# Optimization experiments

Hardware: AMD Instinct MI355X
Metric: run time of the kernel (lower is better)

## Reference

```python
import jax, jax.numpy as jnp
import numpy as np

N = 100000   # nodes
E = 1600000  # edges
IN = 128     # input feature dim
HID = 64     # hidden = IN // 2
OUT = 8      # output_size
B = 16384    # lookup batch


def sage_conv(x, src, dst, W_l, W_r, b, n):
    # PyG SAGEConv (aggr='mean', root_weight=True):
    # out = lin_l(mean_{j in N(i)} x_j) + lin_r(x_i)
    msgs = x[src]                                              # [E, F] gather
    agg = jax.ops.segment_sum(msgs, dst, num_segments=n)       # [N, F] scatter-add
    deg = jax.ops.segment_sum(jnp.ones((src.shape[0],), x.dtype), dst, num_segments=n)
    mean = agg / jnp.maximum(deg, 1.0)[:, None]                # zero-degree -> 0
    return mean @ W_l + x @ W_r + b


def setup_inputs() -> dict:
    key = jax.random.key(0)
    ks = jax.random.split(key, 10)
    node_feats = jax.random.normal(ks[0], (N, IN), dtype=jnp.float32)
    edge_index = jax.random.randint(ks[1], (2, E), 0, N, dtype=jnp.int64)
    idx = jax.random.randint(ks[2], (B,), 0, N, dtype=jnp.int64)
    dropout_mask = jax.random.uniform(ks[3], (N, HID), dtype=jnp.float32)
    s1 = 1.0 / np.sqrt(IN)
    s2 = 1.0 / np.sqrt(HID)
    W1_l = jax.random.normal(ks[4], (IN, HID), dtype=jnp.float32) * s1
    W1_r = jax.random.normal(ks[5], (IN, HID), dtype=jnp.float32) * s1
    b1 = jnp.zeros((HID,), dtype=jnp.float32)
    W2_l = jax.random.normal(ks[6], (HID, OUT), dtype=jnp.float32) * s2
    W2_r = jax.random.normal(ks[7], (HID, OUT), dtype=jnp.float32) * s2
    b2 = jnp.zeros((OUT,), dtype=jnp.float32)
    return {"node_feats": node_feats, "edge_index": edge_index, "idx": idx,
            "dropout_mask": dropout_mask, "W1_l": W1_l, "W1_r": W1_r, "b1": b1,
            "W2_l": W2_l, "W2_r": W2_r, "b2": b2}


def reference(node_feats, edge_index, idx, dropout_mask, W1_l, W1_r, b1, W2_l, W2_r, b2):
    n = node_feats.shape[0]
    src, dst = edge_index[0], edge_index[1]
    h = sage_conv(node_feats, src, dst, W1_l, W1_r, b1, n)     # [N, HID]
    h = jax.nn.relu(h)
    keep = (dropout_mask > 0.5).astype(h.dtype)                # F.dropout p=0.5
    h = h * keep * 2.0                                         # inverted dropout scale 1/(1-p)
    emb = sage_conv(h, src, dst, W2_l, W2_r, b2, n)            # [N, OUT]
    return emb[idx]                                            # [B, OUT]
```

## Files before the change

### kernel.cpp

```cpp
#include <hip/hip_runtime.h>
#include <hip/hip_fp16.h>

#define IN_F 128
#define HID_F 64
#define OUT_F 8

#define BSHIFT 7
#define BGRAN 128
#define BCAP 2688
#define NBUK_MAX 784
#define CHUNK 4096
#define EPT (CHUNK / 256)
#define CEPT ((BCAP + 255) / 256)

typedef _Float16 f16x8 __attribute__((ext_vector_type(8)));
typedef float f32x4 __attribute__((ext_vector_type(4)));

__global__ __launch_bounds__(256) void prep(
    const float* __restrict__ Wl, const float* __restrict__ Wr,
    _Float16* __restrict__ Wt, int* __restrict__ bcur, int nbuk) {
  int blk = blockIdx.x;
  if (blk < 16) {
    int i = blk * 256 + threadIdx.x;
    int n = i & 127;
    int k4 = (i >> 7) * 4;
    _Float16 hv[4];
#pragma unroll
    for (int j = 0; j < 4; ++j) {
      float v = (n < HID_F) ? Wl[(k4 + j) * HID_F + n]
                            : Wr[(k4 + j) * HID_F + (n - HID_F)];
      hv[j] = (_Float16)v;
    }
    *(uint2*)(Wt + (size_t)n * IN_F + k4) = *(uint2*)hv;
  } else {
    for (int i = threadIdx.x; i < nbuk; i += 256) bcur[i] = i * BCAP;
  }
}

__global__ __launch_bounds__(256) void bucket_scatter(
    const int* __restrict__ src, const int* __restrict__ dst,
    int* __restrict__ bcur, int* __restrict__ ebuf,
    const float* __restrict__ mask, unsigned long long* __restrict__ mbits,
    int n_edges, int n_nodes) {
  __shared__ int hist[NBUK_MAX];
  __shared__ int base[NBUK_MAX];
  int t = threadIdx.x;
  for (int i = t; i < NBUK_MAX; i += 256) hist[i] = 0;
  __syncthreads();
  int e0 = blockIdx.x * CHUNK;
  int pk[EPT];
  int bk[EPT];
  int rk[EPT];
#pragma unroll
  for (int k = 0; k < EPT; ++k) {
    int e = e0 + k * 256 + t;
    if (e < n_edges) {
      int s = src[e];
      int d = dst[e];
      bk[k] = d >> BSHIFT;
      pk[k] = ((d & (BGRAN - 1)) << 24) | s;
      rk[k] = atomicAdd(&hist[bk[k]], 1);
    } else {
      bk[k] = -1;
    }
  }
  __syncthreads();
  for (int i = t; i < NBUK_MAX; i += 256) {
    int c = hist[i];
    base[i] = c ? atomicAdd(&bcur[i], c) : 0;
  }
  __syncthreads();
#pragma unroll
  for (int k = 0; k < EPT; ++k) {
    if (bk[k] >= 0) ebuf[base[bk[k]] + rk[k]] = pk[k];
  }

  int mpb = (n_nodes + (int)gridDim.x - 1) / (int)gridDim.x;
  int nb0 = blockIdx.x * mpb;
  int lim = min(nb0 + mpb, n_nodes);
  int w = t >> 6;
  int ln = t & 63;
  for (int nn = nb0 + w * 4; nn < lim; nn += 16) {
    float m0 = (nn + 0 < lim) ? mask[(size_t)(nn + 0) * HID_F + ln] : 0.f;
    float m1 = (nn + 1 < lim) ? mask[(size_t)(nn + 1) * HID_F + ln] : 0.f;
    float m2 = (nn + 2 < lim) ? mask[(size_t)(nn + 2) * HID_F + ln] : 0.f;
    float m3 = (nn + 3 < lim) ? mask[(size_t)(nn + 3) * HID_F + ln] : 0.f;
    unsigned long long b0 = __ballot(m0 > 0.5f);
    unsigned long long b1 = __ballot(m1 > 0.5f);
    unsigned long long b2 = __ballot(m2 > 0.5f);
    unsigned long long b3 = __ballot(m3 > 0.5f);
    if (ln == 0) {
      if (nn + 0 < lim) mbits[nn + 0] = b0;
      if (nn + 1 < lim) mbits[nn + 1] = b1;
      if (nn + 2 < lim) mbits[nn + 2] = b2;
      if (nn + 3 < lim) mbits[nn + 3] = b3;
    }
  }
}

__global__ __launch_bounds__(256) void bucket_csr(
    const int* __restrict__ ebuf, const int* __restrict__ bcur,
    uint2* __restrict__ nd, int* __restrict__ csr_src, int n_nodes) {
  __shared__ int hist[BGRAN];
  __shared__ int excl_s[BGRAN];
  __shared__ int lds_src[BCAP];
  int b = blockIdx.x;
  int t = threadIdx.x;
  if (t < BGRAN) hist[t] = 0;
  __syncthreads();
  int beg = b * BCAP;
  int cnt = bcur[b] - beg;
  int pk[CEPT];
  int rk[CEPT];
#pragma unroll
  for (int u = 0; u < CEPT; ++u) {
    int j = t + u * 256;
    if (j < cnt) {
      pk[u] = ebuf[beg + j];
      rk[u] = atomicAdd(&hist[(unsigned)pk[u] >> 24], 1);
    } else {
      pk[u] = -1;
    }
  }
  __syncthreads();
  if (t < 64) {
    int h0 = hist[2 * t];
    int h1 = hist[2 * t + 1];
    int ps = h0 + h1;
#pragma unroll
    for (int dd = 1; dd < 64; dd <<= 1) {
      int u = __shfl_up(ps, dd);
      if (t >= dd) ps += u;
    }
    excl_s[2 * t] = ps - h1 - h0;
    excl_s[2 * t + 1] = ps - h1;
  }
  __syncthreads();
  if (t < BGRAN) {
    int node = b * BGRAN + t;
    if (node < n_nodes)
      nd[node] = make_uint2((unsigned)(beg + excl_s[t]), (unsigned)hist[t]);
  }
#pragma unroll
  for (int u = 0; u < CEPT; ++u) {
    if (pk[u] != -1) {
      int bin = (unsigned)pk[u] >> 24;
      lds_src[excl_s[bin] + rk[u]] = pk[u] & 0xFFFFFF;
    }
  }
  __syncthreads();
  for (int j = t; j < cnt; j += 256) csr_src[beg + j] = lds_src[j];
}

#define K1_ROWS 64
#define XSH 136
__global__ __launch_bounds__(256) void k1_proj(
    const float* __restrict__ x,
    const _Float16* __restrict__ Wt,
    const float* __restrict__ b1,
    __half* __restrict__ y1h,
    __half* __restrict__ r1h,
    int n_nodes) {
  __shared__ _Float16 XS[K1_ROWS * XSH];
  int tid = threadIdx.x;
  int w = tid >> 6;
  int lane = tid & 63;
  int n0 = blockIdx.x * K1_ROWS;
  int m = lane & 15;
  int quad = lane >> 4;

  f16x8 af[2][4];
#pragma unroll
  for (int ti = 0; ti < 2; ++ti) {
    int t = w + ti * 4;
#pragma unroll
    for (int kk = 0; kk < 4; ++kk)
      af[ti][kk] = *(const f16x8*)(Wt + (size_t)(t * 16 + m) * IN_F + kk * 32 + quad * 8);
  }
  float4 b1v = *(const float4*)(b1 + w * 16 + quad * 4);

#pragma unroll
  for (int p = 0; p < 8; ++p) {
    int i = tid + p * 256;
    int row = i >> 5;
    int k4 = (i & 31) * 4;
    int gs = min(n0 + row, n_nodes - 1);
    float4 v = *(const float4*)(x + (size_t)gs * IN_F + k4);
    _Float16 hv[4] = {(_Float16)v.x, (_Float16)v.y, (_Float16)v.z, (_Float16)v.w};
    *(uint2*)&XS[row * XSH + k4] = *(uint2*)hv;
  }
  __syncthreads();

#pragma unroll
  for (int rt = 0; rt < 4; ++rt) {
    f32x4 acc0 = f32x4{0.f, 0.f, 0.f, 0.f};
    f32x4 acc1 = f32x4{0.f, 0.f, 0.f, 0.f};
#pragma unroll
    for (int kk = 0; kk < 4; ++kk) {
      f16x8 bx = *(const f16x8*)&XS[(rt * 16 + m) * XSH + kk * 32 + quad * 8];
      acc0 = __builtin_amdgcn_mfma_f32_16x16x32_f16(af[0][kk], bx, acc0, 0, 0, 0);
      acc1 = __builtin_amdgcn_mfma_f32_16x16x32_f16(af[1][kk], bx, acc1, 0, 0, 0);
    }
    int node = n0 + rt * 16 + m;
    if (node < n_nodes) {
      __half hy[4], hr[4];
#pragma unroll
      for (int r = 0; r < 4; ++r) {
        hy[r] = __float2half(acc0[r]);
        hr[r] = __float2half(acc1[r] + ((const float*)&b1v)[r]);
      }
      *(uint2*)(y1h + (size_t)node * HID_F + w * 16 + quad * 4) = *(uint2*)hy;
      *(uint2*)(r1h + (size_t)node * HID_F + w * 16 + quad * 4) = *(uint2*)hr;
    }
  }
}

__global__ __launch_bounds__(256) void agg1_fused(
    const __half* __restrict__ y1h,
    const __half* __restrict__ r1h,
    const uint2* __restrict__ nd,
    const int* __restrict__ csr_src,
    const unsigned long long* __restrict__ mbits,
    __half* __restrict__ h_h,
    int n_nodes, int npw) {
  int wid = (blockIdx.x * 256 + threadIdx.x) >> 6;
  int lane = threadIdx.x & 63;
  int q = lane >> 4;
  int f4 = lane & 15;
  int n0 = wid * npw;
  if (n0 >= n_nodes) return;
  int nend = min(n0 + npw, n_nodes);
  const char* yb = (const char*)y1h;
  unsigned foff = (unsigned)(f4 * 8);

#define ACCB(g0, g1, g2, g3)                                 \
  {                                                          \
    __half2 hx = *(const __half2*)&(g0).x;                   \
    __half2 hy = *(const __half2*)&(g0).y;                   \
    hx = __hadd2(hx, *(const __half2*)&(g1).x);              \
    hy = __hadd2(hy, *(const __half2*)&(g1).y);              \
    hx = __hadd2(hx, *(const __half2*)&(g2).x);              \
    hy = __hadd2(hy, *(const __half2*)&(g2).y);              \
    hx = __hadd2(hx, *(const __half2*)&(g3).x);              \
    hy = __hadd2(hy, *(const __half2*)&(g3).y);              \
    float2 fx = __half22float2(hx);                          \
    float2 fy = __half22float2(hy);                          \
    a0 += fx.x; a1 += fx.y; a2 += fy.x; a3 += fy.y;          \
  }

  int nu0 = __builtin_amdgcn_readfirstlane(n0);
  uint2 be_c = nd[nu0];
  unsigned pidx[4] = {0u, 0u, 0u, 0u};
  {
    int d0 = (int)be_c.y;
    if (d0 > 0) {
      const int* cp0 = csr_src + (int)be_c.x;
      int dm = d0 - 1;
#pragma unroll
      for (int k = 0; k < 4; ++k)
        pidx[k] = (unsigned)cp0[min(4 * k + q, dm)];
    }
  }

  for (int n = n0; n < nend; ++n) {
    int nu = __builtin_amdgcn_readfirstlane(n);
    unsigned long long mb = mbits[nu];
    size_t o = (size_t)nu * HID_F + f4 * 4;
    uint2 rg = *(const uint2*)(r1h + o);
    uint2 be_n = make_uint2(0u, 0u);
    if (n + 1 < nend) {
      int nun = __builtin_amdgcn_readfirstlane(n + 1);
      be_n = nd[nun];
    }

    int d = (int)be_c.y;
    const int* cp = csr_src + (int)be_c.x;
    float a0 = 0.f, a1 = 0.f, a2 = 0.f, a3 = 0.f;

    if (d > 0) {
      uint2 g0 = *(const uint2*)(yb + ((pidx[0] << 7) + foff));
      uint2 g1 = *(const uint2*)(yb + ((pidx[1] << 7) + foff));
      uint2 g2 = *(const uint2*)(yb + ((pidx[2] << 7) + foff));
      uint2 g3 = *(const uint2*)(yb + ((pidx[3] << 7) + foff));
      uint2 zz = make_uint2(0u, 0u);
      if (q >= d) g0 = zz;
      if (4 + q >= d) g1 = zz;
      if (8 + q >= d) g2 = zz;
      if (12 + q >= d) g3 = zz;
      ACCB(g0, g1, g2, g3)
    }
    int j = 16;
    for (; j + 16 <= d; j += 16) {
      unsigned s0 = (unsigned)cp[j + q];
      unsigned s1 = (unsigned)cp[j + 4 + q];
      unsigned s2 = (unsigned)cp[j + 8 + q];
      unsigned s3 = (unsigned)cp[j + 12 + q];
      uint2 g0 = *(const uint2*)(yb + ((s0 << 7) + foff));
      uint2 g1 = *(const uint2*)(yb + ((s1 << 7) + foff));
      uint2 g2 = *(const uint2*)(yb + ((s2 << 7) + foff));
      uint2 g3 = *(const uint2*)(yb + ((s3 << 7) + foff));
      ACCB(g0, g1, g2, g3)
    }
    if (j < d) {
      int dm = d - 1;
      int e0 = j + q, e1 = j + 4 + q, e2 = j + 8 + q, e3 = j + 12 + q;
      unsigned s0 = (unsigned)cp[min(e0, dm)];
      unsigned s1 = (unsigned)cp[min(e1, dm)];
      unsigned s2 = (unsigned)cp[min(e2, dm)];
      unsigned s3 = (unsigned)cp[min(e3, dm)];
      uint2 g0 = *(const uint2*)(yb + ((s0 << 7) + foff));
      uint2 g1 = *(const uint2*)(yb + ((s1 << 7) + foff));
      uint2 g2 = *(const uint2*)(yb + ((s2 << 7) + foff));
      uint2 g3 = *(const uint2*)(yb + ((s3 << 7) + foff));
      uint2 zz = make_uint2(0u, 0u);
      if (e0 >= d) g0 = zz;
      if (e1 >= d) g1 = zz;
      if (e2 >= d) g2 = zz;
      if (e3 >= d) g3 = zz;
      ACCB(g0, g1, g2, g3)
    }

    if (n + 1 < nend) {
      int dn = (int)be_n.y;
      if (dn > 0) {
        const int* cpn = csr_src + (int)be_n.x;
        int dmn = dn - 1;
#pragma unroll
        for (int k = 0; k < 4; ++k)
          pidx[k] = (unsigned)cpn[min(4 * k + q, dmn)];
      }
    }

    a0 += __shfl_xor(a0, 16); a0 += __shfl_xor(a0, 32);
    a1 += __shfl_xor(a1, 16); a1 += __shfl_xor(a1, 32);
    a2 += __shfl_xor(a2, 16); a2 += __shfl_xor(a2, 32);
    a3 += __shfl_xor(a3, 16); a3 += __shfl_xor(a3, 32);
    if (q == 0) {
      float inv = 1.0f / fmaxf((float)d, 1.0f);
      float2 r01 = __half22float2(*(const __half2*)&rg.x);
      float2 r23 = __half22float2(*(const __half2*)&rg.y);
      float vx = fmaxf(a0 * inv + r01.x, 0.f);
      float vy = fmaxf(a1 * inv + r01.y, 0.f);
      float vz = fmaxf(a2 * inv + r23.x, 0.f);
      float vw = fmaxf(a3 * inv + r23.y, 0.f);
      int fb = f4 * 4;
      vx = ((mb >> (fb + 0)) & 1ull) ? vx * 2.f : 0.f;
      vy = ((mb >> (fb + 1)) & 1ull) ? vy * 2.f : 0.f;
      vz = ((mb >> (fb + 2)) & 1ull) ? vz * 2.f : 0.f;
      vw = ((mb >> (fb + 3)) & 1ull) ? vw * 2.f : 0.f;
      __half hh[4] = {__float2half(vx), __float2half(vy),
                      __float2half(vz), __float2half(vw)};
      *(uint2*)(h_h + o) = *(uint2*)hh;
    }
    be_c = be_n;
  }
#undef ACCB
}

__global__ __launch_bounds__(256) void k3b_z(
    const __half* __restrict__ h_h,
    const float* __restrict__ W2l,
    __half* __restrict__ z,
    int n_nodes) {
  __shared__ float WS[HID_F][OUT_F];
  int tid = threadIdx.x;
  if (tid < 128) {
    float4 w = *(const float4*)(W2l + tid * 4);
    *(float4*)&WS[tid >> 1][(tid & 1) * 4] = w;
  }
  __syncthreads();
  int node = blockIdx.x * blockDim.x + tid;
  if (node >= n_nodes) return;
  const __half* hr = h_h + (size_t)node * HID_F;
  float acc[8] = {0, 0, 0, 0, 0, 0, 0, 0};
  for (int k = 0; k < HID_F; k += 8) {
    uint4 hv = *(const uint4*)(hr + k);
    float2 f0 = __half22float2(*(const __half2*)&hv.x);
    float2 f1 = __half22float2(*(const __half2*)&hv.y);
    float2 f2 = __half22float2(*(const __half2*)&hv.z);
    float2 f3 = __half22float2(*(const __half2*)&hv.w);
    float hh[8] = {f0.x, f0.y, f1.x, f1.y, f2.x, f2.y, f3.x, f3.y};
#pragma unroll
    for (int j = 0; j < 8; ++j) {
      float4 w0 = *(const float4*)&WS[k + j][0];
      float4 w1 = *(const float4*)&WS[k + j][4];
      acc[0] += hh[j] * w0.x; acc[1] += hh[j] * w0.y;
      acc[2] += hh[j] * w0.z; acc[3] += hh[j] * w0.w;
      acc[4] += hh[j] * w1.x; acc[5] += hh[j] * w1.y;
      acc[6] += hh[j] * w1.z; acc[7] += hh[j] * w1.w;
    }
  }
  __half hz[8];
#pragma unroll
  for (int j = 0; j < 8; ++j) hz[j] = __float2half(acc[j]);
  *(uint4*)(z + (size_t)node * OUT_F) = *(uint4*)hz;
}

__global__ __launch_bounds__(256) void out_fused(
    const int* __restrict__ idx,
    const __half* __restrict__ z,
    const uint2* __restrict__ nd,
    const int* __restrict__ csr_src,
    const __half* __restrict__ h_h,
    const float* __restrict__ W2r,
    const float* __restrict__ b2,
    float* __restrict__ out,
    int n_batch) {
  int b = (blockIdx.x * blockDim.x + threadIdx.x) >> 6;
  int lane = threadIdx.x & 63;
  if (b >= n_batch) return;
  int bu = __builtin_amdgcn_readfirstlane(b);
  int i = idx[bu];
  int iu = __builtin_amdgcn_readfirstlane(i);
  int e8 = lane >> 3;
  int o = lane & 7;
  uint2 be = nd[iu];
  uint4 hv = *(const uint4*)(h_h + (size_t)iu * HID_F + e8 * 8);
  int beg = (int)be.x;
  int d = (int)be.y;
  const int* cp = csr_src + beg;
  const char* zb = (const char*)z;
  unsigned ooff = (unsigned)(o * 2);
  float acc = 0.f;
  int j = e8;
  for (; j + 8 < d; j += 16) {
    unsigned s0 = (unsigned)cp[j];
    unsigned s1 = (unsigned)cp[j + 8];
    float z0 = __half2float(*(const __half*)(zb + ((s0 << 4) + ooff)));
    float z1 = __half2float(*(const __half*)(zb + ((s1 << 4) + ooff)));
    acc += z0 + z1;
  }
  if (j < d) {
    unsigned s0 = (unsigned)cp[j];
    acc += __half2float(*(const __half*)(zb + ((s0 << 4) + ooff)));
  }
  float dv = fmaxf((float)d, 1.0f);
  float v = acc / dv;
  float2 f0 = __half22float2(*(const __half2*)&hv.x);
  float2 f1 = __half22float2(*(const __half2*)&hv.y);
  float2 f2 = __half22float2(*(const __half2*)&hv.z);
  float2 f3 = __half22float2(*(const __half2*)&hv.w);
  float hh[8] = {f0.x, f0.y, f1.x, f1.y, f2.x, f2.y, f3.x, f3.y};
#pragma unroll
  for (int jj = 0; jj < 8; ++jj) {
    int k = e8 * 8 + jj;
    v += hh[jj] * W2r[k * OUT_F + o];
  }
  v += __shfl_xor(v, 8);
  v += __shfl_xor(v, 16);
  v += __shfl_xor(v, 32);
  if (e8 == 0) out[(size_t)b * OUT_F + o] = v + b2[o];
}

extern "C" void kernel_launch(void* const* d_in, const int* in_sizes, int n_in,
                              void* d_out, int out_size, void* d_ws, size_t ws_size,
                              hipStream_t stream) {
  const float* x    = (const float*)d_in[0];
  const int*   ei   = (const int*)d_in[1];
  const int*   idx  = (const int*)d_in[2];
  const float* mask = (const float*)d_in[3];
  const float* W1l  = (const float*)d_in[4];
  const float* W1r  = (const float*)d_in[5];
  const float* b1   = (const float*)d_in[6];
  const float* W2l  = (const float*)d_in[7];
  const float* W2r  = (const float*)d_in[8];
  const float* b2   = (const float*)d_in[9];
  float* out = (float*)d_out;

  int n_nodes = in_sizes[0] / IN_F;
  int n_edges = in_sizes[1] / 2;
  int n_batch = in_sizes[2];
  const int* src = ei;
  const int* dst = ei + n_edges;

  int nbuk = (n_nodes + BGRAN - 1) / BGRAN;
  int nchunk = (n_edges + CHUNK - 1) / CHUNK;

  char* ws = (char*)d_ws;
  size_t off = 0;
  __half* y1h = (__half*)(ws + off); off += (size_t)n_nodes * HID_F * 2;
  __half* r1h = (__half*)(ws + off); off += (size_t)n_nodes * HID_F * 2;
  __half* h_h = (__half*)(ws + off); off += (size_t)n_nodes * HID_F * 2;
  __half* z   = (__half*)(ws + off); off += (size_t)n_nodes * OUT_F * 2;
  unsigned long long* mbits = (unsigned long long*)(ws + off); off += (size_t)n_nodes * 8;
  _Float16* Wt = (_Float16*)(ws + off); off += (size_t)IN_F * IN_F * 2;
  int* ebuf    = (int*)(ws + off); off += (size_t)nbuk * BCAP * 4;
  int* csr_src = (int*)(ws + off); off += (size_t)nbuk * BCAP * 4;
  uint2* nd    = (uint2*)(ws + off); off += (size_t)n_nodes * 8;
  int* bcur    = (int*)(ws + off); off += NBUK_MAX * 4;

  prep<<<17, 256, 0, stream>>>(W1l, W1r, Wt, bcur, nbuk);
  bucket_scatter<<<nchunk, 256, 0, stream>>>(src, dst, bcur, ebuf,
                                             mask, mbits, n_edges, n_nodes);
  k1_proj<<<(n_nodes + K1_ROWS - 1) / K1_ROWS, 256, 0, stream>>>(
      x, Wt, b1, y1h, r1h, n_nodes);
  bucket_csr<<<nbuk, 256, 0, stream>>>(ebuf, bcur, nd, csr_src, n_nodes);

  {
    int tw = 8192;
    int npw = (n_nodes + tw - 1) / tw;
    int nw = (n_nodes + npw - 1) / npw;
    int blocks = (nw + 3) / 4;
    agg1_fused<<<blocks, 256, 0, stream>>>(
        y1h, r1h, nd, csr_src, mbits, h_h, n_nodes, npw);
  }

  k3b_z<<<(n_nodes + 255) / 256, 256, 0, stream>>>(h_h, W2l, z, n_nodes);
  {
    long long th = (long long)n_batch * 64;
    out_fused<<<(int)((th + 255) / 256), 256, 0, stream>>>(
        idx, z, nd, csr_src, h_h, W2r, b2, out, n_batch);
  }
}
```

Measured before the change: 236.3 us.

## Process two nodes per wave in agg1 and move mask packing to bucket_csr

Result: slower. 247.6 us (+4.8%).

```diff
diff --git a/kernel.cpp b/kernel.cpp
--- a/kernel.cpp
+++ b/kernel.cpp
@@ -9,7 +9,7 @@
 #define BGRAN 128
 #define BCAP 2688
 #define NBUK_MAX 784
-#define CHUNK 4096
+#define CHUNK 2048
 #define EPT (CHUNK / 256)
 #define CEPT ((BCAP + 255) / 256)
 
@@ -39,9 +39,7 @@
 
 __global__ __launch_bounds__(256) void bucket_scatter(
     const int* __restrict__ src, const int* __restrict__ dst,
-    int* __restrict__ bcur, int* __restrict__ ebuf,
-    const float* __restrict__ mask, unsigned long long* __restrict__ mbits,
-    int n_edges, int n_nodes) {
+    int* __restrict__ bcur, int* __restrict__ ebuf, int n_edges) {
   __shared__ int hist[NBUK_MAX];
   __shared__ int base[NBUK_MAX];
   int t = threadIdx.x;
@@ -74,33 +72,13 @@
   for (int k = 0; k < EPT; ++k) {
     if (bk[k] >= 0) ebuf[base[bk[k]] + rk[k]] = pk[k];
   }
-
-  int mpb = (n_nodes + (int)gridDim.x - 1) / (int)gridDim.x;
-  int nb0 = blockIdx.x * mpb;
-  int lim = min(nb0 + mpb, n_nodes);
-  int w = t >> 6;
-  int ln = t & 63;
-  for (int nn = nb0 + w * 4; nn < lim; nn += 16) {
-    float m0 = (nn + 0 < lim) ? mask[(size_t)(nn + 0) * HID_F + ln] : 0.f;
-    float m1 = (nn + 1 < lim) ? mask[(size_t)(nn + 1) * HID_F + ln] : 0.f;
-    float m2 = (nn + 2 < lim) ? mask[(size_t)(nn + 2) * HID_F + ln] : 0.f;
-    float m3 = (nn + 3 < lim) ? mask[(size_t)(nn + 3) * HID_F + ln] : 0.f;
-    unsigned long long b0 = __ballot(m0 > 0.5f);
-    unsigned long long b1 = __ballot(m1 > 0.5f);
-    unsigned long long b2 = __ballot(m2 > 0.5f);
-    unsigned long long b3 = __ballot(m3 > 0.5f);
-    if (ln == 0) {
-      if (nn + 0 < lim) mbits[nn + 0] = b0;
-      if (nn + 1 < lim) mbits[nn + 1] = b1;
-      if (nn + 2 < lim) mbits[nn + 2] = b2;
-      if (nn + 3 < lim) mbits[nn + 3] = b3;
-    }
-  }
 }
 
 __global__ __launch_bounds__(256) void bucket_csr(
     const int* __restrict__ ebuf, const int* __restrict__ bcur,
-    uint2* __restrict__ nd, int* __restrict__ csr_src, int n_nodes) {
+    uint2* __restrict__ nd, int* __restrict__ csr_src,
+    const float* __restrict__ mask, unsigned long long* __restrict__ mbits,
+    int n_nodes) {
   __shared__ int hist[BGRAN];
   __shared__ int excl_s[BGRAN];
   __shared__ int lds_src[BCAP];
@@ -150,6 +128,31 @@
   }
   __syncthreads();
   for (int j = t; j < cnt; j += 256) csr_src[beg + j] = lds_src[j];
+
+  {
+    int w = t >> 6;
+    int ln = t & 63;
+    int nb0 = b * BGRAN + w * 32;
+    int nlim = min(b * BGRAN + BGRAN, n_nodes);
+#pragma unroll
+    for (int u = 0; u < 8; ++u) {
+      int nn = nb0 + u * 4;
+      float m0 = (nn + 0 < nlim) ? mask[(size_t)(nn + 0) * HID_F + ln] : 0.f;
+      float m1 = (nn + 1 < nlim) ? mask[(size_t)(nn + 1) * HID_F + ln] : 0.f;
+      float m2 = (nn + 2 < nlim) ? mask[(size_t)(nn + 2) * HID_F + ln] : 0.f;
+      float m3 = (nn + 3 < nlim) ? mask[(size_t)(nn + 3) * HID_F + ln] : 0.f;
+      unsigned long long b0 = __ballot(m0 > 0.5f);
+      unsigned long long b1 = __ballot(m1 > 0.5f);
+      unsigned long long b2 = __ballot(m2 > 0.5f);
+      unsigned long long b3 = __ballot(m3 > 0.5f);
+      if (ln == 0) {
+        if (nn + 0 < nlim) mbits[nn + 0] = b0;
+        if (nn + 1 < nlim) mbits[nn + 1] = b1;
+        if (nn + 2 < nlim) mbits[nn + 2] = b2;
+        if (nn + 3 < nlim) mbits[nn + 3] = b3;
+      }
+    }
+  }
 }
 
 #define K1_ROWS 64
@@ -212,6 +215,97 @@
       *(uint2*)(y1h + (size_t)node * HID_F + w * 16 + quad * 4) = *(uint2*)hy;
       *(uint2*)(r1h + (size_t)node * HID_F + w * 16 + quad * 4) = *(uint2*)hr;
     }
+  }
+}
+
+__device__ __forceinline__ void load_pidx(unsigned* pidx, uint2 be,
+                                          const int* __restrict__ csr_src,
+                                          int q) {
+  int dd = (int)be.y;
+  if (dd > 0) {
+    const int* cp_ = csr_src + (int)be.x;
+    int dm_ = dd - 1;
+#pragma unroll
+    for (int k = 0; k < 8; ++k)
+      pidx[k] = (unsigned)cp_[min(4 * k + q, dm_)];
+  } else {
+#pragma unroll
+    for (int k = 0; k < 8; ++k) pidx[k] = 0u;
+  }
+}
+
+__device__ __forceinline__ void gather8(uint2* g, const unsigned* pidx,
+                                        const char* __restrict__ yb,
+                                        unsigned foff, int d) {
+  uint2 zz = make_uint2(0u, 0u);
+#pragma unroll
+  for (int k = 0; k < 4; ++k)
+    g[k] = *(const uint2*)(yb + ((pidx[k] << 7) + foff));
+  if (d > 16) {
+#pragma unroll
+    for (int k = 4; k < 8; ++k)
+      g[k] = *(const uint2*)(yb + ((pidx[k] << 7) + foff));
+  } else {
+#pragma unroll
+    for (int k = 4; k < 8; ++k) g[k] = zz;
+  }
+}
+
+__device__ __forceinline__ void accum8(const uint2* g, int d, int q,
+                                       float& a0, float& a1,
+                                       float& a2, float& a3) {
+  unsigned zi = 0u;
+  __half2 hx = *(const __half2*)&zi;
+  __half2 hy = *(const __half2*)&zi;
+#pragma unroll
+  for (int k = 0; k < 4; ++k) {
+    uint2 gk = (4 * k + q < d) ? g[k] : make_uint2(0u, 0u);
+    hx = __hadd2(hx, *(const __half2*)&gk.x);
+    hy = __hadd2(hy, *(const __half2*)&gk.y);
+  }
+  float2 fx = __half22float2(hx);
+  float2 fy = __half22float2(hy);
+  a0 += fx.x; a1 += fx.y; a2 += fy.x; a3 += fy.y;
+  if (d > 16) {
+    __half2 ux = *(const __half2*)&zi;
+    __half2 uy = *(const __half2*)&zi;
+#pragma unroll
+    for (int k = 4; k < 8; ++k) {
+      uint2 gk = (4 * k + q < d) ? g[k] : make_uint2(0u, 0u);
+      ux = __hadd2(ux, *(const __half2*)&gk.x);
+      uy = __hadd2(uy, *(const __half2*)&gk.y);
+    }
+    float2 gx = __half22float2(ux);
+    float2 gy = __half22float2(uy);
+    a0 += gx.x; a1 += gx.y; a2 += gy.x; a3 += gy.y;
+  }
+}
+
+__device__ __forceinline__ void reduce_epi(float a0, float a1, float a2,
+                                           float a3, int d, uint2 rg,
+                                           unsigned long long mb, size_t o,
+                                           int q, int f4,
+                                           __half* __restrict__ h_h) {
+  a0 += __shfl_xor(a0, 16); a0 += __shfl_xor(a0, 32);
+  a1 += __shfl_xor(a1, 16); a1 += __shfl_xor(a1, 32);
+  a2 += __shfl_xor(a2, 16); a2 += __shfl_xor(a2, 32);
+  a3 += __shfl_xor(a3, 16); a3 += __shfl_xor(a3, 32);
+  if (q == 0) {
+    float inv = 1.0f / fmaxf((float)d, 1.0f);
+    float2 r01 = __half22float2(*(const __half2*)&rg.x);
+    float2 r23 = __half22float2(*(const __half2*)&rg.y);
+    float vx = fmaxf(a0 * inv + r01.x, 0.f);
+    float vy = fmaxf(a1 * inv + r01.y, 0.f);
+    float vz = fmaxf(a2 * inv + r23.x, 0.f);
+    float vw = fmaxf(a3 * inv + r23.y, 0.f);
+    int fb = f4 * 4;
+    vx = ((mb >> (fb + 0)) & 1ull) ? vx * 2.f : 0.f;
+    vy = ((mb >> (fb + 1)) & 1ull) ? vy * 2.f : 0.f;
+    vz = ((mb >> (fb + 2)) & 1ull) ? vz * 2.f : 0.f;
+    vw = ((mb >> (fb + 3)) & 1ull) ? vw * 2.f : 0.f;
+    __half hh[4] = {__float2half(vx), __float2half(vy),
+                    __float2half(vz), __float2half(vw)};
+    *(uint2*)(h_h + o) = *(uint2*)hh;
   }
 }
 
@@ -233,128 +327,122 @@
   const char* yb = (const char*)y1h;
   unsigned foff = (unsigned)(f4 * 8);
 
-#define ACCB(g0, g1, g2, g3)                                 \
-  {                                                          \
-    __half2 hx = *(const __half2*)&(g0).x;                   \
-    __half2 hy = *(const __half2*)&(g0).y;                   \
-    hx = __hadd2(hx, *(const __half2*)&(g1).x);              \
-    hy = __hadd2(hy, *(const __half2*)&(g1).y);              \
-    hx = __hadd2(hx, *(const __half2*)&(g2).x);              \
-    hy = __hadd2(hy, *(const __half2*)&(g2).y);              \
-    hx = __hadd2(hx, *(const __half2*)&(g3).x);              \
-    hy = __hadd2(hy, *(const __half2*)&(g3).y);              \
-    float2 fx = __half22float2(hx);                          \
-    float2 fy = __half22float2(hy);                          \
-    a0 += fx.x; a1 += fx.y; a2 += fy.x; a3 += fy.y;          \
-  }
-
-  int nu0 = __builtin_amdgcn_readfirstlane(n0);
-  uint2 be_c = nd[nu0];
-  unsigned pidx[4] = {0u, 0u, 0u, 0u};
-  {
-    int d0 = (int)be_c.y;
-    if (d0 > 0) {
-      const int* cp0 = csr_src + (int)be_c.x;
-      int dm = d0 - 1;
-#pragma unroll
-      for (int k = 0; k < 4; ++k)
-        pidx[k] = (unsigned)cp0[min(4 * k + q, dm)];
-    }
-  }
-
-  for (int n = n0; n < nend; ++n) {
-    int nu = __builtin_amdgcn_readfirstlane(n);
-    unsigned long long mb = mbits[nu];
-    size_t o = (size_t)nu * HID_F + f4 * 4;
-    uint2 rg = *(const uint2*)(r1h + o);
-    uint2 be_n = make_uint2(0u, 0u);
-    if (n + 1 < nend) {
-      int nun = __builtin_amdgcn_readfirstlane(n + 1);
-      be_n = nd[nun];
-    }
-
-    int d = (int)be_c.y;
-    const int* cp = csr_src + (int)be_c.x;
+  uint2 beA = nd[__builtin_amdgcn_readfirstlane(n0)];
+  uint2 beB = make_uint2(0u, 0u);
+  if (n0 + 1 < nend) beB = nd[__builtin_amdgcn_readfirstlane(n0 + 1)];
+  unsigned pA[8], pB[8];
+  load_pidx(pA, beA, csr_src, q);
+  load_pidx(pB, beB, csr_src, q);
+
+  for (int n = n0; n < nend; n += 2) {
+    bool has2 = (n + 1 < nend);
+    int dA = (int)beA.y;
+    int dB = (int)beB.y;
+    int nuA = __builtin_amdgcn_readfirstlane(n);
+
+    unsigned long long mbA = mbits[nuA];
+    size_t oA = (size_t)nuA * HID_F + f4 * 4;
+    uint2 rgA = *(const uint2*)(r1h + oA);
+    unsigned long long mbB = 0ull;
+    size_t oB = 0;
+    uint2 rgB = make_uint2(0u, 0u);
+    if (has2) {
+      int nuB = __builtin_amdgcn_readfirstlane(n + 1);
+      mbB = mbits[nuB];
+      oB = (size_t)nuB * HID_F + f4 * 4;
+      rgB = *(const uint2*)(r1h + oB);
+    }
+    uint2 gA[8], gB[8];
+    gather8(gA, pA, yb, foff, dA);
+    if (has2) gather8(gB, pB, yb, foff, dB);
+    uint2 beC = make_uint2(0u, 0u), beD = make_uint2(0u, 0u);
+    if (n + 2 < nend) beC = nd[__builtin_amdgcn_readfirstlane(n + 2)];
+    if (n + 3 < nend) beD = nd[__builtin_amdgcn_readfirstlane(n + 3)];
+
     float a0 = 0.f, a1 = 0.f, a2 = 0.f, a3 = 0.f;
-
-    if (d > 0) {
-      uint2 g0 = *(const uint2*)(yb + ((pidx[0] << 7) + foff));
-      uint2 g1 = *(const uint2*)(yb + ((pidx[1] << 7) + foff));
-      uint2 g2 = *(const uint2*)(yb + ((pidx[2] << 7) + foff));
-      uint2 g3 = *(const uint2*)(yb + ((pidx[3] << 7) + foff));
-      uint2 zz = make_uint2(0u, 0u);
-      if (q >= d) g0 = zz;
-      if (4 + q >= d) g1 = zz;
-      if (8 + q >= d) g2 = zz;
-      if (12 + q >= d) g3 = zz;
-      ACCB(g0, g1, g2, g3)
-    }
-    int j = 16;
-    for (; j + 16 <= d; j += 16) {
-      unsigned s0 = (unsigned)cp[j + q];
-      unsigned s1 = (unsigned)cp[j + 4 + q];
-      unsigned s2 = (unsigned)cp[j + 8 + q];
-      unsigned s3 = (unsigned)cp[j + 12 + q];
-      uint2 g0 = *(const uint2*)(yb + ((s0 << 7) + foff));
-      uint2 g1 = *(const uint2*)(yb + ((s1 << 7) + foff));
-      uint2 g2 = *(const uint2*)(yb + ((s2 << 7) + foff));
-      uint2 g3 = *(const uint2*)(yb + ((s3 << 7) + foff));
-      ACCB(g0, g1, g2, g3)
-    }
-    if (j < d) {
-      int dm = d - 1;
-      int e0 = j + q, e1 = j + 4 + q, e2 = j + 8 + q, e3 = j + 12 + q;
-      unsigned s0 = (unsigned)cp[min(e0, dm)];
-      unsigned s1 = (unsigned)cp[min(e1, dm)];
-      unsigned s2 = (unsigned)cp[min(e2, dm)];
-      unsigned s3 = (unsigned)cp[min(e3, dm)];
-      uint2 g0 = *(const uint2*)(yb + ((s0 << 7) + foff));
-      uint2 g1 = *(const uint2*)(yb + ((s1 << 7) + foff));
-      uint2 g2 = *(const uint2*)(yb + ((s2 << 7) + foff));
-      uint2 g3 = *(const uint2*)(yb + ((s3 << 7) + foff));
-      uint2 zz = make_uint2(0u, 0u);
-      if (e0 >= d) g0 = zz;
-      if (e1 >= d) g1 = zz;
-      if (e2 >= d) g2 = zz;
-      if (e3 >= d) g3 = zz;
-      ACCB(g0, g1, g2, g3)
-    }
-
-    if (n + 1 < nend) {
-      int dn = (int)be_n.y;
-      if (dn > 0) {
-        const int* cpn = csr_src + (int)be_n.x;
-        int dmn = dn - 1;
-#pragma unroll
-        for (int k = 0; k < 4; ++k)
-          pidx[k] = (unsigned)cpn[min(4 * k + q, dmn)];
+    accum8(gA, dA, q, a0, a1, a2, a3);
+    if (dA > 32) {
+      const int* cp = csr_src + (int)beA.x;
+      int dm = dA - 1;
+      for (int j = 32; j < dA; j += 16) {
+        int e0 = j + q, e1 = j + 4 + q, e2 = j + 8 + q, e3 = j + 12 + q;
+        unsigned s0 = (unsigned)cp[min(e0, dm)];
+        unsigned s1 = (unsigned)cp[min(e1, dm)];
+        unsigned s2 = (unsigned)cp[min(e2, dm)];
+        unsigned s3 = (unsigned)cp[min(e3, dm)];
+        uint2 t0 = *(const uint2*)(yb + ((s0 << 7) + foff));
+        uint2 t1 = *(const uint2*)(yb + ((s1 << 7) + foff));
+        uint2 t2 = *(const uint2*)(yb + ((s2 << 7) + foff));
+        uint2 t3 = *(const uint2*)(yb + ((s3 << 7) + foff));
+        uint2 zz = make_uint2(0u, 0u);
+        if (e0 >= dA) t0 = zz;
+        if (e1 >= dA) t1 = zz;
+        if (e2 >= dA) t2 = zz;
+        if (e3 >= dA) t3 = zz;
+        unsigned zi = 0u;
+        __half2 hx = *(const __half2*)&zi;
+        __half2 hy = *(const __half2*)&zi;
+        hx = __hadd2(hx, *(const __half2*)&t0.x);
+        hy = __hadd2(hy, *(const __half2*)&t0.y);
+        hx = __hadd2(hx, *(const __half2*)&t1.x);
+        hy = __hadd2(hy, *(const __half2*)&t1.y);
+        hx = __hadd2(hx, *(const __half2*)&t2.x);
+        hy = __hadd2(hy, *(const __half2*)&t2.y);
+        hx = __hadd2(hx, *(const __half2*)&t3.x);
+        hy = __hadd2(hy, *(const __half2*)&t3.y);
+        float2 fx = __half22float2(hx);
+        float2 fy = __half22float2(hy);
+        a0 += fx.x; a1 += fx.y; a2 += fy.x; a3 += fy.y;
       }
     }
-
-    a0 += __shfl_xor(a0, 16); a0 += __shfl_xor(a0, 32);
-    a1 += __shfl_xor(a1, 16); a1 += __shfl_xor(a1, 32);
-    a2 += __shfl_xor(a2, 16); a2 += __shfl_xor(a2, 32);
-    a3 += __shfl_xor(a3, 16); a3 += __shfl_xor(a3, 32);
-    if (q == 0) {
-      float inv = 1.0f / fmaxf((float)d, 1.0f);
-      float2 r01 = __half22float2(*(const __half2*)&rg.x);
-      float2 r23 = __half22float2(*(const __half2*)&rg.y);
-      float vx = fmaxf(a0 * inv + r01.x, 0.f);
-      float vy = fmaxf(a1 * inv + r01.y, 0.f);
-      float vz = fmaxf(a2 * inv + r23.x, 0.f);
-      float vw = fmaxf(a3 * inv + r23.y, 0.f);
-      int fb = f4 * 4;
-      vx = ((mb >> (fb + 0)) & 1ull) ? vx * 2.f : 0.f;
-      vy = ((mb >> (fb + 1)) & 1ull) ? vy * 2.f : 0.f;
-      vz = ((mb >> (fb + 2)) & 1ull) ? vz * 2.f : 0.f;
-      vw = ((mb >> (fb + 3)) & 1ull) ? vw * 2.f : 0.f;
-      __half hh[4] = {__float2half(vx), __float2half(vy),
-                      __float2half(vz), __float2half(vw)};
-      *(uint2*)(h_h + o) = *(uint2*)hh;
-    }
-    be_c = be_n;
-  }
-#undef ACCB
+    float b0 = 0.f, b1 = 0.f, b2 = 0.f, b3 = 0.f;
+    if (has2) {
+      accum8(gB, dB, q, b0, b1, b2, b3);
+      if (dB > 32) {
+        const int* cp = csr_src + (int)beB.x;
+        int dm = dB - 1;
+        for (int j = 32; j < dB; j += 16) {
+          int e0 = j + q, e1 = j + 4 + q, e2 = j + 8 + q, e3 = j + 12 + q;
+          unsigned s0 = (unsigned)cp[min(e0, dm)];
+          unsigned s1 = (unsigned)cp[min(e1, dm)];
+          unsigned s2 = (unsigned)cp[min(e2, dm)];
+          unsigned s3 = (unsigned)cp[min(e3, dm)];
+          uint2 t0 = *(const uint2*)(yb + ((s0 << 7) + foff));
+          uint2 t1 = *(const uint2*)(yb + ((s1 << 7) + foff));
+          uint2 t2 = *(const uint2*)(yb + ((s2 << 7) + foff));
+          uint2 t3 = *(const uint2*)(yb + ((s3 << 7) + foff));
+          uint2 zz = make_uint2(0u, 0u);
+          if (e0 >= dB) t0 = zz;
+          if (e1 >= dB) t1 = zz;
+          if (e2 >= dB) t2 = zz;
+          if (e3 >= dB) t3 = zz;
+          unsigned zi = 0u;
+          __half2 hx = *(const __half2*)&zi;
+          __half2 hy = *(const __half2*)&zi;
+          hx = __hadd2(hx, *(const __half2*)&t0.x);
+          hy = __hadd2(hy, *(const __half2*)&t0.y);
+          hx = __hadd2(hx, *(const __half2*)&t1.x);
+          hy = __hadd2(hy, *(const __half2*)&t1.y);
+          hx = __hadd2(hx, *(const __half2*)&t2.x);
+          hy = __hadd2(hy, *(const __half2*)&t2.y);
+          hx = __hadd2(hx, *(const __half2*)&t3.x);
+          hy = __hadd2(hy, *(const __half2*)&t3.y);
+          float2 fx = __half22float2(hx);
+          float2 fy = __half22float2(hy);
+          b0 += fx.x; b1 += fx.y; b2 += fy.x; b3 += fy.y;
+        }
+      }
+    }
+
+    load_pidx(pA, beC, csr_src, q);
+    load_pidx(pB, beD, csr_src, q);
+
+    reduce_epi(a0, a1, a2, a3, dA, rgA, mbA, oA, q, f4, h_h);
+    if (has2) reduce_epi(b0, b1, b2, b3, dB, rgB, mbB, oB, q, f4, h_h);
+
+    beA = beC;
+    beB = beD;
+  }
 }
 
 __global__ __launch_bounds__(256) void k3b_z(
@@ -490,14 +578,14 @@
   int* bcur    = (int*)(ws + off); off += NBUK_MAX * 4;
 
   prep<<<17, 256, 0, stream>>>(W1l, W1r, Wt, bcur, nbuk);
-  bucket_scatter<<<nchunk, 256, 0, stream>>>(src, dst, bcur, ebuf,
-                                             mask, mbits, n_edges, n_nodes);
+  bucket_scatter<<<nchunk, 256, 0, stream>>>(src, dst, bcur, ebuf, n_edges);
   k1_proj<<<(n_nodes + K1_ROWS - 1) / K1_ROWS, 256, 0, stream>>>(
       x, Wt, b1, y1h, r1h, n_nodes);
-  bucket_csr<<<nbuk, 256, 0, stream>>>(ebuf, bcur, nd, csr_src, n_nodes);
+  bucket_csr<<<nbuk, 256, 0, stream>>>(ebuf, bcur, nd, csr_src,
+                                       mask, mbits, n_nodes);
 
   {
-    int tw = 8192;
+    int tw = 16384;
     int npw = (n_nodes + tw - 1) / tw;
     int nw = (n_nodes + npw - 1) / npw;
     int blocks = (nw + 3) / 4;
```

## Fuse second-layer projection and dropout mask into first aggregation kernel

Applied to the files above, without the earlier changes.

New measurement: 239.0 us. Within noise of the previous version (+1.2%).

```diff
diff --git a/kernel.cpp b/kernel.cpp
--- a/kernel.cpp
+++ b/kernel.cpp
@@ -9,7 +9,7 @@
 #define BGRAN 128
 #define BCAP 2688
 #define NBUK_MAX 784
-#define CHUNK 4096
+#define CHUNK 2048
 #define EPT (CHUNK / 256)
 #define CEPT ((BCAP + 255) / 256)
 
@@ -39,9 +39,7 @@
 
 __global__ __launch_bounds__(256) void bucket_scatter(
     const int* __restrict__ src, const int* __restrict__ dst,
-    int* __restrict__ bcur, int* __restrict__ ebuf,
-    const float* __restrict__ mask, unsigned long long* __restrict__ mbits,
-    int n_edges, int n_nodes) {
+    int* __restrict__ bcur, int* __restrict__ ebuf, int n_edges) {
   __shared__ int hist[NBUK_MAX];
   __shared__ int base[NBUK_MAX];
   int t = threadIdx.x;
@@ -73,28 +71,6 @@
 #pragma unroll
   for (int k = 0; k < EPT; ++k) {
     if (bk[k] >= 0) ebuf[base[bk[k]] + rk[k]] = pk[k];
-  }
-
-  int mpb = (n_nodes + (int)gridDim.x - 1) / (int)gridDim.x;
-  int nb0 = blockIdx.x * mpb;
-  int lim = min(nb0 + mpb, n_nodes);
-  int w = t >> 6;
-  int ln = t & 63;
-  for (int nn = nb0 + w * 4; nn < lim; nn += 16) {
-    float m0 = (nn + 0 < lim) ? mask[(size_t)(nn + 0) * HID_F + ln] : 0.f;
-    float m1 = (nn + 1 < lim) ? mask[(size_t)(nn + 1) * HID_F + ln] : 0.f;
-    float m2 = (nn + 2 < lim) ? mask[(size_t)(nn + 2) * HID_F + ln] : 0.f;
-    float m3 = (nn + 3 < lim) ? mask[(size_t)(nn + 3) * HID_F + ln] : 0.f;
-    unsigned long long b0 = __ballot(m0 > 0.5f);
-    unsigned long long b1 = __ballot(m1 > 0.5f);
-    unsigned long long b2 = __ballot(m2 > 0.5f);
-    unsigned long long b3 = __ballot(m3 > 0.5f);
-    if (ln == 0) {
-      if (nn + 0 < lim) mbits[nn + 0] = b0;
-      if (nn + 1 < lim) mbits[nn + 1] = b1;
-      if (nn + 2 < lim) mbits[nn + 2] = b2;
-      if (nn + 3 < lim) mbits[nn + 3] = b3;
-    }
   }
 }
 
@@ -220,8 +196,10 @@
     const __half* __restrict__ r1h,
     const uint2* __restrict__ nd,
     const int* __restrict__ csr_src,
-    const unsigned long long* __restrict__ mbits,
+    const float* __restrict__ mask,
+    const float* __restrict__ W2l,
     __half* __restrict__ h_h,
+    __half* __restrict__ z,
     int n_nodes, int npw) {
   int wid = (blockIdx.x * 256 + threadIdx.x) >> 6;
   int lane = threadIdx.x & 63;
@@ -232,6 +210,13 @@
   int nend = min(n0 + npw, n_nodes);
   const char* yb = (const char*)y1h;
   unsigned foff = (unsigned)(f4 * 8);
+
+  float wz0[4], wz1[4];
+#pragma unroll
+  for (int j = 0; j < 4; ++j) {
+    wz0[j] = W2l[(f4 * 4 + j) * OUT_F + 2 * q];
+    wz1[j] = W2l[(f4 * 4 + j) * OUT_F + 2 * q + 1];
+  }
 
 #define ACCB(g0, g1, g2, g3)                                 \
   {                                                          \
@@ -248,8 +233,7 @@
     a0 += fx.x; a1 += fx.y; a2 += fy.x; a3 += fy.y;          \
   }
 
-  int nu0 = __builtin_amdgcn_readfirstlane(n0);
-  uint2 be_c = nd[nu0];
+  uint2 be_c = nd[__builtin_amdgcn_readfirstlane(n0)];
   unsigned pidx[4] = {0u, 0u, 0u, 0u};
   {
     int d0 = (int)be_c.y;
@@ -264,9 +248,9 @@
 
   for (int n = n0; n < nend; ++n) {
     int nu = __builtin_amdgcn_readfirstlane(n);
-    unsigned long long mb = mbits[nu];
     size_t o = (size_t)nu * HID_F + f4 * 4;
     uint2 rg = *(const uint2*)(r1h + o);
+    float4 mrow = *(const float4*)(mask + o);
     uint2 be_n = make_uint2(0u, 0u);
     if (n + 1 < nend) {
       int nun = __builtin_amdgcn_readfirstlane(n + 1);
@@ -335,65 +319,37 @@
     a1 += __shfl_xor(a1, 16); a1 += __shfl_xor(a1, 32);
     a2 += __shfl_xor(a2, 16); a2 += __shfl_xor(a2, 32);
     a3 += __shfl_xor(a3, 16); a3 += __shfl_xor(a3, 32);
-    if (q == 0) {
-      float inv = 1.0f / fmaxf((float)d, 1.0f);
-      float2 r01 = __half22float2(*(const __half2*)&rg.x);
-      float2 r23 = __half22float2(*(const __half2*)&rg.y);
-      float vx = fmaxf(a0 * inv + r01.x, 0.f);
-      float vy = fmaxf(a1 * inv + r01.y, 0.f);
-      float vz = fmaxf(a2 * inv + r23.x, 0.f);
-      float vw = fmaxf(a3 * inv + r23.y, 0.f);
-      int fb = f4 * 4;
-      vx = ((mb >> (fb + 0)) & 1ull) ? vx * 2.f : 0.f;
-      vy = ((mb >> (fb + 1)) & 1ull) ? vy * 2.f : 0.f;
-      vz = ((mb >> (fb + 2)) & 1ull) ? vz * 2.f : 0.f;
-      vw = ((mb >> (fb + 3)) & 1ull) ? vw * 2.f : 0.f;
-      __half hh[4] = {__float2half(vx), __float2half(vy),
-                      __float2half(vz), __float2half(vw)};
-      *(uint2*)(h_h + o) = *(uint2*)hh;
+
+    float inv = 1.0f / fmaxf((float)d, 1.0f);
+    float2 r01 = __half22float2(*(const __half2*)&rg.x);
+    float2 r23 = __half22float2(*(const __half2*)&rg.y);
+    float vx = fmaxf(a0 * inv + r01.x, 0.f);
+    float vy = fmaxf(a1 * inv + r01.y, 0.f);
+    float vz = fmaxf(a2 * inv + r23.x, 0.f);
+    float vw = fmaxf(a3 * inv + r23.y, 0.f);
+    vx = (mrow.x > 0.5f) ? vx * 2.f : 0.f;
+    vy = (mrow.y > 0.5f) ? vy * 2.f : 0.f;
+    vz = (mrow.z > 0.5f) ? vz * 2.f : 0.f;
+    vw = (mrow.w > 0.5f) ? vw * 2.f : 0.f;
+    __half hh[4] = {__float2half(vx), __float2half(vy),
+                    __float2half(vz), __float2half(vw)};
+    if (q == 0) *(uint2*)(h_h + o) = *(uint2*)hh;
+
+    float hq[4] = {__half2float(hh[0]), __half2float(hh[1]),
+                   __half2float(hh[2]), __half2float(hh[3])};
+    float p0 = hq[0] * wz0[0] + hq[1] * wz0[1] + hq[2] * wz0[2] + hq[3] * wz0[3];
+    float p1 = hq[0] * wz1[0] + hq[1] * wz1[1] + hq[2] * wz1[2] + hq[3] * wz1[3];
+    p0 += __shfl_xor(p0, 1); p0 += __shfl_xor(p0, 2);
+    p0 += __shfl_xor(p0, 4); p0 += __shfl_xor(p0, 8);
+    p1 += __shfl_xor(p1, 1); p1 += __shfl_xor(p1, 2);
+    p1 += __shfl_xor(p1, 4); p1 += __shfl_xor(p1, 8);
+    if (f4 == 0) {
+      __half zp[2] = {__float2half(p0), __float2half(p1)};
+      *(uint*)((char*)z + (size_t)nu * OUT_F * 2 + q * 4) = *(uint*)zp;
     }
     be_c = be_n;
   }
 #undef ACCB
-}
-
-__global__ __launch_bounds__(256) void k3b_z(
-    const __half* __restrict__ h_h,
-    const float* __restrict__ W2l,
-    __half* __restrict__ z,
-    int n_nodes) {
-  __shared__ float WS[HID_F][OUT_F];
-  int tid = threadIdx.x;
-  if (tid < 128) {
-    float4 w = *(const float4*)(W2l + tid * 4);
-    *(float4*)&WS[tid >> 1][(tid & 1) * 4] = w;
-  }
-  __syncthreads();
-  int node = blockIdx.x * blockDim.x + tid;
-  if (node >= n_nodes) return;
-  const __half* hr = h_h + (size_t)node * HID_F;
-  float acc[8] = {0, 0, 0, 0, 0, 0, 0, 0};
-  for (int k = 0; k < HID_F; k += 8) {
-    uint4 hv = *(const uint4*)(hr + k);
-    float2 f0 = __half22float2(*(const __half2*)&hv.x);
-    float2 f1 = __half22float2(*(const __half2*)&hv.y);
-    float2 f2 = __half22float2(*(const __half2*)&hv.z);
-    float2 f3 = __half22float2(*(const __half2*)&hv.w);
-    float hh[8] = {f0.x, f0.y, f1.x, f1.y, f2.x, f2.y, f3.x, f3.y};
-#pragma unroll
-    for (int j = 0; j < 8; ++j) {
-      float4 w0 = *(const float4*)&WS[k + j][0];
-      float4 w1 = *(const float4*)&WS[k + j][4];
-      acc[0] += hh[j] * w0.x; acc[1] += hh[j] * w0.y;
-      acc[2] += hh[j] * w0.z; acc[3] += hh[j] * w0.w;
-      acc[4] += hh[j] * w1.x; acc[5] += hh[j] * w1.y;
-      acc[6] += hh[j] * w1.z; acc[7] += hh[j] * w1.w;
-    }
-  }
-  __half hz[8];
-#pragma unroll
-  for (int j = 0; j < 8; ++j) hz[j] = __float2half(acc[j]);
-  *(uint4*)(z + (size_t)node * OUT_F) = *(uint4*)hz;
 }
 
 __global__ __launch_bounds__(256) void out_fused(
@@ -482,7 +438,6 @@
   __half* r1h = (__half*)(ws + off); off += (size_t)n_nodes * HID_F * 2;
   __half* h_h = (__half*)(ws + off); off += (size_t)n_nodes * HID_F * 2;
   __half* z   = (__half*)(ws + off); off += (size_t)n_nodes * OUT_F * 2;
-  unsigned long long* mbits = (unsigned long long*)(ws + off); off += (size_t)n_nodes * 8;
   _Float16* Wt = (_Float16*)(ws + off); off += (size_t)IN_F * IN_F * 2;
   int* ebuf    = (int*)(ws + off); off += (size_t)nbuk * BCAP * 4;
   int* csr_src = (int*)(ws + off); off += (size_t)nbuk * BCAP * 4;
@@ -490,8 +445,7 @@
   int* bcur    = (int*)(ws + off); off += NBUK_MAX * 4;
 
   prep<<<17, 256, 0, stream>>>(W1l, W1r, Wt, bcur, nbuk);
-  bucket_scatter<<<nchunk, 256, 0, stream>>>(src, dst, bcur, ebuf,
-                                             mask, mbits, n_edges, n_nodes);
+  bucket_scatter<<<nchunk, 256, 0, stream>>>(src, dst, bcur, ebuf, n_edges);
   k1_proj<<<(n_nodes + K1_ROWS - 1) / K1_ROWS, 256, 0, stream>>>(
       x, Wt, b1, y1h, r1h, n_nodes);
   bucket_csr<<<nbuk, 256, 0, stream>>>(ebuf, bcur, nd, csr_src, n_nodes);
@@ -502,10 +456,9 @@
     int nw = (n_nodes + npw - 1) / npw;
     int blocks = (nw + 3) / 4;
     agg1_fused<<<blocks, 256, 0, stream>>>(
-        y1h, r1h, nd, csr_src, mbits, h_h, n_nodes, npw);
-  }
-
-  k3b_z<<<(n_nodes + 255) / 256, 256, 0, stream>>>(h_h, W2l, z, n_nodes);
+        y1h, r1h, nd, csr_src, mask, W2l, h_h, z, n_nodes, npw);
+  }
+
   {
     long long th = (long long)n_batch * 64;
     out_fused<<<(int)((th + 255) / 256), 256, 0, stream>>>(
```

## Move dropout-mask bit packing into projection kernel and halve scatter chunk

Applied to the files above, without the earlier changes.

Measured after the change: 237.3 us. About the same (+0.4%).

```diff
diff --git a/kernel.cpp b/kernel.cpp
--- a/kernel.cpp
+++ b/kernel.cpp
@@ -9,7 +9,7 @@
 #define BGRAN 128
 #define BCAP 2688
 #define NBUK_MAX 784
-#define CHUNK 4096
+#define CHUNK 2048
 #define EPT (CHUNK / 256)
 #define CEPT ((BCAP + 255) / 256)
 
@@ -39,9 +39,7 @@
 
 __global__ __launch_bounds__(256) void bucket_scatter(
     const int* __restrict__ src, const int* __restrict__ dst,
-    int* __restrict__ bcur, int* __restrict__ ebuf,
-    const float* __restrict__ mask, unsigned long long* __restrict__ mbits,
-    int n_edges, int n_nodes) {
+    int* __restrict__ bcur, int* __restrict__ ebuf, int n_edges) {
   __shared__ int hist[NBUK_MAX];
   __shared__ int base[NBUK_MAX];
   int t = threadIdx.x;
@@ -74,28 +72,6 @@
   for (int k = 0; k < EPT; ++k) {
     if (bk[k] >= 0) ebuf[base[bk[k]] + rk[k]] = pk[k];
   }
-
-  int mpb = (n_nodes + (int)gridDim.x - 1) / (int)gridDim.x;
-  int nb0 = blockIdx.x * mpb;
-  int lim = min(nb0 + mpb, n_nodes);
-  int w = t >> 6;
-  int ln = t & 63;
-  for (int nn = nb0 + w * 4; nn < lim; nn += 16) {
-    float m0 = (nn + 0 < lim) ? mask[(size_t)(nn + 0) * HID_F + ln] : 0.f;
-    float m1 = (nn + 1 < lim) ? mask[(size_t)(nn + 1) * HID_F + ln] : 0.f;
-    float m2 = (nn + 2 < lim) ? mask[(size_t)(nn + 2) * HID_F + ln] : 0.f;
-    float m3 = (nn + 3 < lim) ? mask[(size_t)(nn + 3) * HID_F + ln] : 0.f;
-    unsigned long long b0 = __ballot(m0 > 0.5f);
-    unsigned long long b1 = __ballot(m1 > 0.5f);
-    unsigned long long b2 = __ballot(m2 > 0.5f);
-    unsigned long long b3 = __ballot(m3 > 0.5f);
-    if (ln == 0) {
-      if (nn + 0 < lim) mbits[nn + 0] = b0;
-      if (nn + 1 < lim) mbits[nn + 1] = b1;
-      if (nn + 2 < lim) mbits[nn + 2] = b2;
-      if (nn + 3 < lim) mbits[nn + 3] = b3;
-    }
-  }
 }
 
 __global__ __launch_bounds__(256) void bucket_csr(
@@ -158,8 +134,10 @@
     const float* __restrict__ x,
     const _Float16* __restrict__ Wt,
     const float* __restrict__ b1,
+    const float* __restrict__ mask,
     __half* __restrict__ y1h,
     __half* __restrict__ r1h,
+    unsigned long long* __restrict__ mbits,
     int n_nodes) {
   __shared__ _Float16 XS[K1_ROWS * XSH];
   int tid = threadIdx.x;
@@ -169,6 +147,13 @@
   int m = lane & 15;
   int quad = lane >> 4;
 
+  float mv[16];
+#pragma unroll
+  for (int u = 0; u < 16; ++u) {
+    int node = n0 + w * 16 + u;
+    mv[u] = (node < n_nodes) ? mask[(size_t)node * HID_F + lane] : 0.f;
+  }
+
   f16x8 af[2][4];
 #pragma unroll
   for (int ti = 0; ti < 2; ++ti) {
@@ -212,6 +197,13 @@
       *(uint2*)(y1h + (size_t)node * HID_F + w * 16 + quad * 4) = *(uint2*)hy;
       *(uint2*)(r1h + (size_t)node * HID_F + w * 16 + quad * 4) = *(uint2*)hr;
     }
+  }
+
+#pragma unroll
+  for (int u = 0; u < 16; ++u) {
+    int node = n0 + w * 16 + u;
+    unsigned long long bb = __ballot(mv[u] > 0.5f);
+    if (lane == 0 && node < n_nodes) mbits[node] = bb;
   }
 }
 
@@ -248,8 +240,7 @@
     a0 += fx.x; a1 += fx.y; a2 += fy.x; a3 += fy.y;          \
   }
 
-  int nu0 = __builtin_amdgcn_readfirstlane(n0);
-  uint2 be_c = nd[nu0];
+  uint2 be_c = nd[__builtin_amdgcn_readfirstlane(n0)];
   unsigned pidx[4] = {0u, 0u, 0u, 0u};
   {
     int d0 = (int)be_c.y;
@@ -490,10 +481,9 @@
   int* bcur    = (int*)(ws + off); off += NBUK_MAX * 4;
 
   prep<<<17, 256, 0, stream>>>(W1l, W1r, Wt, bcur, nbuk);
-  bucket_scatter<<<nchunk, 256, 0, stream>>>(src, dst, bcur, ebuf,
-                                             mask, mbits, n_edges, n_nodes);
+  bucket_scatter<<<nchunk, 256, 0, stream>>>(src, dst, bcur, ebuf, n_edges);
   k1_proj<<<(n_nodes + K1_ROWS - 1) / K1_ROWS, 256, 0, stream>>>(
-      x, Wt, b1, y1h, r1h, n_nodes);
+      x, Wt, b1, mask, y1h, r1h, mbits, n_nodes);
   bucket_csr<<<nbuk, 256, 0, stream>>>(ebuf, bcur, nd, csr_src, n_nodes);
 
   {
```
